# Kernel optimization log

Measured on AMD Instinct MI355X. Metric: run time of the kernel, lower is better.

The kernel has to match this reference:

```python
import jax, jax.numpy as jnp
import numpy as np
import math

B, S, D, H = 4, 2048, 1024, 16
HD = D // H  # head dim = 64


def setup_inputs() -> dict:
    key = jax.random.key(0)
    ks = jax.random.split(key, 8)
    queries = jax.random.normal(ks[0], (B, S, D), dtype=jnp.float32)
    keys = jax.random.normal(ks[1], (B, S, D), dtype=jnp.float32)
    values = jax.random.normal(ks[2], (B, S, D), dtype=jnp.float32)
    valid_lens = jnp.maximum(jax.random.randint(ks[3], (B,), 0, S), 1).astype(jnp.int64)
    scale = 1.0 / math.sqrt(D)
    Wq = jax.random.normal(ks[4], (H, D, HD), dtype=jnp.float32) * scale
    Wk = jax.random.normal(ks[5], (H, D, HD), dtype=jnp.float32) * scale
    Wv = jax.random.normal(ks[6], (H, D, HD), dtype=jnp.float32) * scale
    Wo = jax.random.normal(ks[7], (H * HD, D), dtype=jnp.float32) * scale
    return {"queries": queries, "keys": keys, "values": values,
            "valid_lens": valid_lens, "Wq": Wq, "Wk": Wk, "Wv": Wv, "Wo": Wo}


def reference(queries, keys, values, valid_lens, Wq, Wk, Wv, Wo):
    # Per-head projections, batched over heads: [B,S,D] x [H,D,HD] -> [B,H,S,HD]
    q = jnp.einsum('bsd,hde->bhse', queries, Wq)
    k = jnp.einsum('bsd,hde->bhse', keys, Wk)
    v = jnp.einsum('bsd,hde->bhse', values, Wv)
    # Scaled dot-product scores: [B,H,S,S]
    scores = jnp.einsum('bhse,bhte->bhst', q, k) / jnp.sqrt(jnp.float32(HD))
    # Padding mask only (causal=False default in the torch forward)
    pad = jnp.arange(S)[None, :] >= valid_lens[:, None]  # [B,S] True = masked
    scores = jnp.where(pad[:, None, None, :], -jnp.inf, scores)
    attn = jax.nn.softmax(scores, axis=-1)
    out = jnp.einsum('bhst,bhte->bhse', attn, v)  # [B,H,S,HD]
    out = out.transpose(0, 2, 1, 3).reshape(q.shape[0], S, H * HD)  # concat heads
    return out @ Wo
```

## Files before the change

kernel.cpp:

```cpp
#include <hip/hip_runtime.h>
#include <hip/hip_bf16.h>

typedef __bf16 bf16;
typedef __attribute__((ext_vector_type(8))) __bf16 bf16x8;
typedef __attribute__((ext_vector_type(4))) float f32x4;

#define DEV __device__ __forceinline__

DEV float fexp2(float x) {
#if __has_builtin(__builtin_amdgcn_exp2f)
  return __builtin_amdgcn_exp2f(x);
#else
  return exp2f(x);
#endif
}

DEV void gload_lds16(const void* g, void* l) {
  __builtin_amdgcn_global_load_lds(
      (__attribute__((address_space(1))) void*)(g),
      (__attribute__((address_space(3))) void*)(l), 16, 0, 0);
}

template <int N>
DEV void waitvm() { asm volatile("s_waitcnt vmcnt(%0)" ::"n"(N) : "memory"); }
DEV void fence() { asm volatile("" ::: "memory"); }
DEV void bar() { fence(); __builtin_amdgcn_s_barrier(); fence(); }

__global__ void k_cvt_all(const float* __restrict__ q, const float* __restrict__ k,
                          const float* __restrict__ v, const float* __restrict__ Wq,
                          const float* __restrict__ Wk, const float* __restrict__ Wv,
                          const float* __restrict__ Wo, bf16* __restrict__ qb,
                          bf16* __restrict__ kb, bf16* __restrict__ vb,
                          bf16* __restrict__ WqkvT, bf16* __restrict__ WoT) {
  const int bid = blockIdx.x;
  if (bid < 12288) {
    const int which = bid >> 12;
    const float* in = which == 0 ? q : which == 1 ? k : v;
    bf16* out = which == 0 ? qb : which == 1 ? kb : vb;
    const int i = (bid & 4095) * 256 + threadIdx.x;
    const float4* p = reinterpret_cast<const float4*>(in) + (size_t)i * 2;
    float4 a = p[0], b = p[1];
    bf16x8 o;
    o[0] = (bf16)a.x; o[1] = (bf16)a.y; o[2] = (bf16)a.z; o[3] = (bf16)a.w;
    o[4] = (bf16)b.x; o[5] = (bf16)b.y; o[6] = (bf16)b.z; o[7] = (bf16)b.w;
    *reinterpret_cast<bf16x8*>(out + (size_t)i * 8) = o;
  } else {
    const int idx = (bid - 12288) * 256 + threadIdx.x;
    const int which = idx >> 20, r = idx & ((1 << 20) - 1);
    if (which < 3) {
      const float* W = which == 0 ? Wq : which == 1 ? Wk : Wv;
      const int d = r & 1023, n = r >> 10;
      float val = W[((size_t)(n >> 6) << 16) + (size_t)d * 64 + (n & 63)];
      if (which == 0) val *= 0.180336880f;
      WqkvT[((size_t)which << 20) + r] = (bf16)val;
    } else {
      const int kk = r & 1023, n = r >> 10;
      WoT[r] = (bf16)Wo[(size_t)kk * 1024 + n];
    }
  }
}

DEV void stageA(const bf16* __restrict__ Am, bf16 (*lds)[64], int k0, int tid) {
  const int wv = tid >> 6;
#pragma unroll
  for (int l = 0; l < 2; ++l) {
    const int row = l * 64 + (tid >> 3);
    const int e = (((tid & 7) ^ (row & 7)) << 3);
    gload_lds16(Am + (size_t)row * 1024 + k0 + e,
                (char*)lds + l * 8192 + wv * 1024);
  }
}
DEV void stageBh(const bf16* __restrict__ Bt, bf16 (*lds)[64], int h, int k0, int tid) {
  const int wv = tid >> 6;
#pragma unroll
  for (int l = 0; l < 2; ++l) {
    const int row = h * 128 + l * 64 + (tid >> 3);
    const int e = (((tid & 7) ^ (row & 7)) << 3);
    gload_lds16(Bt + (size_t)row * 1024 + k0 + e,
                (char*)lds + h * 16384 + l * 8192 + wv * 1024);
  }
}
DEV bf16x8 ldsfrag(const bf16 (*lds)[64], int row, int kk, int lgrp) {
  const int ch = ((kk << 2) + lgrp) ^ (row & 7);
  return *reinterpret_cast<const bf16x8*>((const char*)&lds[row][0] + (ch << 4));
}

#define GEMM_KLOOP(Am, Bt, acc)                                               \
  stageA(Am, AsB[0], 0, tid);                                                 \
  stageBh(Bt, BsB[0], 0, 0, tid);                                             \
  stageBh(Bt, BsB[0], 1, 0, tid);                                             \
  stageBh(Bt, BsB[1], 0, 64, tid);                                            \
  stageBh(Bt, BsB[1], 1, 64, tid);                                            \
  waitvm<4>();                                                                \
  bar();                                                                      \
  int cur = 0;                                                                \
  for (int kt = 0; kt < NT; ++kt) {                                           \
    bf16x8 bfr[4][2], afr[2][2];                                              \
    _Pragma("unroll") for (int n = 0; n < 4; ++n)                             \
        _Pragma("unroll") for (int kk = 0; kk < 2; ++kk)                      \
            bfr[n][kk] = ldsfrag(BsB[cur], wn * 64 + n * 16 + lid, kk, lgrp); \
    _Pragma("unroll") for (int mi = 0; mi < 2; ++mi)                          \
        _Pragma("unroll") for (int kk = 0; kk < 2; ++kk)                      \
            afr[mi][kk] = ldsfrag(AsB[cur], wr * 64 + mi * 16 + lid, kk, lgrp); \
    if (kt + 1 < NT) stageA(Am, AsB[cur ^ 1], (kt + 1) * 64, tid);            \
    bar();                                                                    \
    __builtin_amdgcn_s_setprio(1);                                            \
    _Pragma("unroll") for (int mi = 0; mi < 2; ++mi)                          \
        _Pragma("unroll") for (int n = 0; n < 4; ++n)                         \
            _Pragma("unroll") for (int kk = 0; kk < 2; ++kk)                  \
                acc[mi][n] = __builtin_amdgcn_mfma_f32_16x16x32_bf16(         \
                    afr[mi][kk], bfr[n][kk], acc[mi][n], 0, 0, 0);            \
    __builtin_amdgcn_s_setprio(0);                                            \
    bar();                                                                    \
    _Pragma("unroll") for (int mi = 0; mi < 2; ++mi)                          \
        _Pragma("unroll") for (int kk = 0; kk < 2; ++kk)                      \
            afr[mi][kk] = ldsfrag(AsB[cur], wr * 64 + (2 + mi) * 16 + lid, kk, lgrp); \
    if (kt + 2 < NT) {                                                        \
      stageBh(Bt, BsB[cur], 0, (kt + 2) * 64, tid);                           \
      stageBh(Bt, BsB[cur], 1, (kt + 2) * 64, tid);                           \
    }                                                                         \
    bar();                                                                    \
    __builtin_amdgcn_s_setprio(1);                                            \
    _Pragma("unroll") for (int mi = 0; mi < 2; ++mi)                          \
        _Pragma("unroll") for (int n = 0; n < 4; ++n)                         \
            _Pragma("unroll") for (int kk = 0; kk < 2; ++kk)                  \
                acc[2 + mi][n] = __builtin_amdgcn_mfma_f32_16x16x32_bf16(     \
                    afr[mi][kk], bfr[n][kk], acc[2 + mi][n], 0, 0, 0);        \
    __builtin_amdgcn_s_setprio(0);                                            \
    if (kt < NT - 2) waitvm<4>();                                             \
    else if (kt == NT - 2) waitvm<0>();                                       \
    bar();                                                                    \
    cur ^= 1;                                                                 \
  }

__global__ __launch_bounds__(512, 2) void k_gemm_qkv(const bf16* __restrict__ qA,
                                                     const bf16* __restrict__ kA,
                                                     const bf16* __restrict__ vA,
                                                     const bf16* __restrict__ Wt,
                                                     bf16* __restrict__ Qh,
                                                     bf16* __restrict__ Kh,
                                                     bf16* __restrict__ Vt) {
  __shared__ __align__(16) bf16 AsB[2][128][64];
  __shared__ __align__(16) bf16 BsB[2][256][64];
  const int tid = threadIdx.x, lane = tid & 63, w = tid >> 6;
  const int lgrp = lane >> 4, lid = lane & 15;
  const int wr = w >> 2, wn = w & 3;
  const int bid0 = blockIdx.x;
  const int bid = (bid0 & 7) * 96 + (bid0 >> 3);
  const int proj = bid >> 8;
  const int local = bid & 255;
  const int mt = local >> 2, ntl = local & 3;
  const int m0 = mt * 128, n0 = ntl * 256;
  const bf16* A = proj == 0 ? qA : proj == 1 ? kA : vA;
  const bf16* Am = A + (size_t)m0 * 1024;
  const bf16* Bt = Wt + ((size_t)proj * 1024 + n0) * 1024;

  f32x4 acc[4][4] = {};
  constexpr int NT = 16;
  GEMM_KLOOP(Am, Bt, acc)

  const int hh = (n0 >> 6) + wn;
  if (proj == 0) {
#pragma unroll
    for (int mm = 0; mm < 4; ++mm) {
      const int rowb = m0 + wr * 64 + mm * 16 + lgrp * 4;
      const int bb = rowb >> 11, s = rowb & 2047;
#pragma unroll
      for (int n = 0; n < 4; ++n) {
        const int e = n * 16 + lid;
        bf16* dst = Qh + (((size_t)bb * 16 + hh) * 2048 + s) * 64 + e;
#pragma unroll
        for (int r = 0; r < 4; ++r) dst[(size_t)r * 64] = (bf16)acc[mm][n][r];
      }
    }
  } else if (proj == 1) {
#pragma unroll
    for (int mm = 0; mm < 4; ++mm) {
      const int rowb = m0 + wr * 64 + mm * 16 + lgrp * 4;
      const int bb = rowb >> 11, s = rowb & 2047;
#pragma unroll
      for (int n = 0; n < 4; ++n) {
        const int e = n * 16 + lid;
#pragma unroll
        for (int r = 0; r < 4; ++r) {
          const int sr = s + r;
          Kh[(((size_t)bb * 16 + hh) * 2048 + sr) * 64 + (e ^ ((sr & 7) << 3))] =
              (bf16)acc[mm][n][r];
        }
      }
    }
  } else {
#pragma unroll
    for (int mm = 0; mm < 4; ++mm) {
      const int rowb = m0 + wr * 64 + mm * 16 + lgrp * 4;
      const int bb = rowb >> 11, s = rowb & 2047;
#pragma unroll
      for (int n = 0; n < 4; ++n) {
        const int e = n * 16 + lid;
        union { bf16 hv[4]; uint2 u; } tmp;
#pragma unroll
        for (int r = 0; r < 4; ++r) tmp.hv[r] = (bf16)acc[mm][n][r];
        bf16* dst = Vt + (((size_t)bb * 16 + hh) * 64 + e) * 2048 + (s ^ ((e & 7) << 3));
        *reinterpret_cast<uint2*>(dst) = tmp.u;
      }
    }
  }
}

__global__ __launch_bounds__(512, 2) void k_gemm_out8(const bf16* __restrict__ A,
                                                      const bf16* __restrict__ Wo,
                                                      float* __restrict__ C) {
  __shared__ __align__(16) bf16 AsB[2][128][64];
  __shared__ __align__(16) bf16 BsB[2][256][64];
  const int tid = threadIdx.x, lane = tid & 63, w = tid >> 6;
  const int lgrp = lane >> 4, lid = lane & 15;
  const int wr = w >> 2, wn = w & 3;
  const int bid0 = blockIdx.x;
  const int bid = (bid0 & 7) * 32 + (bid0 >> 3);
  const int mt = bid >> 2, ntl = bid & 3;
  const int m0 = mt * 128, n0 = ntl * 256;
  const bf16* Am = A + (size_t)m0 * 1024;
  const bf16* Bt = Wo + (size_t)n0 * 1024;

  f32x4 acc[4][4] = {};
  constexpr int NT = 16;
  GEMM_KLOOP(Am, Bt, acc)

#pragma unroll
  for (int mm = 0; mm < 4; ++mm) {
    const int rowb = m0 + wr * 64 + mm * 16 + lgrp * 4;
#pragma unroll
    for (int n = 0; n < 4; ++n) {
      const int col = n0 + wn * 64 + n * 16 + lid;
#pragma unroll
      for (int r = 0; r < 4; ++r)
        C[(size_t)(rowb + r) * 1024 + col] = acc[mm][n][r];
    }
  }
}

__global__ __launch_bounds__(256, 3) void k_flash(const bf16* __restrict__ Qh,
                                                  const bf16* __restrict__ Ksw,
                                                  const bf16* __restrict__ Vsw,
                                                  const int* __restrict__ valid,
                                                  bf16* __restrict__ Ob) {
  __shared__ __align__(16) char Ks[2][8192];
  __shared__ __align__(16) char Vs[2][8192];
  __shared__ __align__(16) char Plds[4][4096];
  const int tid = threadIdx.x, lane = tid & 63, w = tid >> 6;
  const int lgrp = lane >> 4, lid = lane & 15;
  const int blk = blockIdx.x;
  const int qt = blk & 15, bh = blk >> 4;
  const int b = bh >> 4, h = bh & 15;
  const int s0 = qt * 128 + w * 32;
  const bf16* Qp = Qh + ((size_t)bh * 2048 + s0) * 64;
  const bf16* Kp = Ksw + (size_t)bh * 2048 * 64;
  const bf16* Vp = Vsw + (size_t)bh * 64 * 2048;
  const int vl = valid[b];
  const int nt = (vl + 63) >> 6;
  const int full = vl >> 6;

  const int sr0 = 16 * w + (lane >> 3), col8 = (lane & 7) * 8;

  gload_lds16(Kp + (size_t)sr0 * 64 + col8, &Ks[0][(16 * w) * 128]);
  gload_lds16(Kp + (size_t)(sr0 + 8) * 64 + col8, &Ks[0][(16 * w + 8) * 128]);
  gload_lds16(Vp + (size_t)sr0 * 2048 + col8, &Vs[0][(16 * w) * 128]);
  gload_lds16(Vp + (size_t)(sr0 + 8) * 2048 + col8, &Vs[0][(16 * w + 8) * 128]);

  bf16x8 aq[2][2];
#pragma unroll
  for (int g = 0; g < 2; ++g)
#pragma unroll
    for (int c = 0; c < 2; ++c)
      aq[g][c] = *reinterpret_cast<const bf16x8*>(Qp + (g * 16 + lid) * 64 + c * 32 + lgrp * 8);

  f32x4 Of[2][4] = {};
  float mrow[2] = {-1e30f, -1e30f};
  float lpart[2] = {0.f, 0.f};
  char* Pw = &Plds[w][0];
  float* PwF = (float*)Pw;
  const int pswz = (lid & 7) << 4;

  int cur = 0;
  for (int t = 0; t < nt; ++t) {
    const int t0 = t * 64;
    __syncthreads();
    if (t + 1 < nt) {
      const int t1 = t0 + 64;
      gload_lds16(Kp + (size_t)(t1 + sr0) * 64 + col8, &Ks[cur ^ 1][(16 * w) * 128]);
      gload_lds16(Kp + (size_t)(t1 + sr0 + 8) * 64 + col8, &Ks[cur ^ 1][(16 * w + 8) * 128]);
      gload_lds16(Vp + (size_t)sr0 * 2048 + t1 + col8, &Vs[cur ^ 1][(16 * w) * 128]);
      gload_lds16(Vp + (size_t)(sr0 + 8) * 2048 + t1 + col8, &Vs[cur ^ 1][(16 * w + 8) * 128]);
    }
    f32x4 sc[2][4] = {{}, {}};
#pragma unroll
    for (int kk = 0; kk < 2; ++kk) {
      bf16x8 bkh[4];
#pragma unroll
      for (int ct = 0; ct < 4; ++ct) {
        const int row = ct * 16 + lid;
        bkh[ct] = *reinterpret_cast<const bf16x8*>(
            &Ks[cur][row * 128] + ((kk * 64 + lgrp * 16) ^ ((row & 7) << 4)));
      }
#pragma unroll
      for (int g = 0; g < 2; ++g)
#pragma unroll
        for (int ct = 0; ct < 4; ++ct)
          sc[g][ct] = __builtin_amdgcn_mfma_f32_16x16x32_bf16(bkh[ct], aq[g][kk],
                                                              sc[g][ct], 0, 0, 0);
    }
    if (t >= full) {
#pragma unroll
      for (int ct = 0; ct < 4; ++ct)
#pragma unroll
        for (int r = 0; r < 4; ++r) {
          const bool m = (t0 + ct * 16 + lgrp * 4 + r) >= vl;
          sc[0][ct][r] = m ? -1e30f : sc[0][ct][r];
          sc[1][ct][r] = m ? -1e30f : sc[1][ct][r];
        }
    }
    float vm[2];
#pragma unroll
    for (int g = 0; g < 2; ++g) {
      float v = fmaxf(fmaxf(fmaxf(sc[g][0][0], sc[g][0][1]), fmaxf(sc[g][0][2], sc[g][0][3])),
                      fmaxf(fmaxf(sc[g][1][0], sc[g][1][1]), fmaxf(sc[g][1][2], sc[g][1][3])));
      v = fmaxf(v, fmaxf(fmaxf(fmaxf(sc[g][2][0], sc[g][2][1]), fmaxf(sc[g][2][2], sc[g][2][3])),
                         fmaxf(fmaxf(sc[g][3][0], sc[g][3][1]), fmaxf(sc[g][3][2], sc[g][3][3]))));
      vm[g] = v;
    }
    if (__any((vm[0] > mrow[0] + 8.f) | (vm[1] > mrow[1] + 8.f))) {
#pragma unroll
      for (int g = 0; g < 2; ++g) {
        float v = vm[g];
        v = fmaxf(v, __shfl_xor(v, 16));
        v = fmaxf(v, __shfl_xor(v, 32));
        float mnew = fmaxf(mrow[g], v);
        float scl = fexp2(mrow[g] - mnew);
        mrow[g] = mnew;
        lpart[g] *= scl;
        if (lgrp == 0) PwF[g * 512 + lid] = scl;
      }
      asm volatile("s_waitcnt lgkmcnt(0)" ::: "memory");
      f32x4 sq0 = *reinterpret_cast<const f32x4*>(PwF + lgrp * 4);
      f32x4 sq1 = *reinterpret_cast<const f32x4*>(PwF + 512 + lgrp * 4);
#pragma unroll
      for (int f = 0; f < 4; ++f)
#pragma unroll
        for (int r = 0; r < 4; ++r) {
          Of[0][f][r] *= sq0[r];
          Of[1][f][r] *= sq1[r];
        }
    }
#pragma unroll
    for (int g = 0; g < 2; ++g)
#pragma unroll
      for (int ct = 0; ct < 4; ++ct)
#pragma unroll
        for (int r = 0; r < 4; ++r)
          sc[g][ct][r] = fexp2(sc[g][ct][r] - mrow[g]);
#pragma unroll
    for (int g = 0; g < 2; ++g)
#pragma unroll
      for (int ct = 0; ct < 4; ++ct) {
        union { bf16 hv[2]; unsigned int u; } p0, p1;
        p0.hv[0] = (bf16)sc[g][ct][0]; p0.hv[1] = (bf16)sc[g][ct][1];
        p1.hv[0] = (bf16)sc[g][ct][2]; p1.hv[1] = (bf16)sc[g][ct][3];
        char* base = Pw + g * 2048 + lid * 128 + ((ct * 32 + lgrp * 8) ^ pswz);
        *reinterpret_cast<unsigned int*>(base) = p0.u;
        *reinterpret_cast<unsigned int*>(base + 4) = p1.u;
      }
    asm volatile("s_waitcnt lgkmcnt(0)" ::: "memory");
    bf16x8 pa[2][2];
#pragma unroll
    for (int g = 0; g < 2; ++g) {
      pa[g][0] = *reinterpret_cast<const bf16x8*>(Pw + g * 2048 + lid * 128 + ((lgrp * 16) ^ pswz));
      pa[g][1] = *reinterpret_cast<const bf16x8*>(Pw + g * 2048 + lid * 128 + ((64 + lgrp * 16) ^ pswz));
    }
#pragma unroll
    for (int f = 0; f < 4; ++f) {
      const int row = f * 16 + lid;
      const char* vb = &Vs[cur][row * 128];
      const int msk = (row & 7) << 4;
      bf16x8 bv0 = *reinterpret_cast<const bf16x8*>(vb + ((lgrp * 16) ^ msk));
      bf16x8 bv1 = *reinterpret_cast<const bf16x8*>(vb + ((64 + lgrp * 16) ^ msk));
      Of[0][f] = __builtin_amdgcn_mfma_f32_16x16x32_bf16(pa[0][0], bv0, Of[0][f], 0, 0, 0);
      Of[0][f] = __builtin_amdgcn_mfma_f32_16x16x32_bf16(pa[0][1], bv1, Of[0][f], 0, 0, 0);
      Of[1][f] = __builtin_amdgcn_mfma_f32_16x16x32_bf16(pa[1][0], bv0, Of[1][f], 0, 0, 0);
      Of[1][f] = __builtin_amdgcn_mfma_f32_16x16x32_bf16(pa[1][1], bv1, Of[1][f], 0, 0, 0);
    }
#pragma unroll
    for (int g = 0; g < 2; ++g)
      lpart[g] += ((sc[g][0][0] + sc[g][0][1]) + (sc[g][0][2] + sc[g][0][3])) +
                  ((sc[g][1][0] + sc[g][1][1]) + (sc[g][1][2] + sc[g][1][3])) +
                  ((sc[g][2][0] + sc[g][2][1]) + (sc[g][2][2] + sc[g][2][3])) +
                  ((sc[g][3][0] + sc[g][3][1]) + (sc[g][3][2] + sc[g][3][3]));
    cur ^= 1;
  }
#pragma unroll
  for (int g = 0; g < 2; ++g) {
    float l = lpart[g];
    l += __shfl_xor(l, 16);
    l += __shfl_xor(l, 32);
    if (lgrp == 0) PwF[g * 512 + lid] = 1.f / l;
  }
  asm volatile("s_waitcnt lgkmcnt(0)" ::: "memory");
  f32x4 iq0 = *reinterpret_cast<const f32x4*>(PwF + lgrp * 4);
  f32x4 iq1 = *reinterpret_cast<const f32x4*>(PwF + 512 + lgrp * 4);
  bf16* Op = Ob + ((size_t)b * 2048 + s0) * 1024 + h * 64;
#pragma unroll
  for (int r = 0; r < 4; ++r)
#pragma unroll
    for (int f = 0; f < 4; ++f) {
      Op[(size_t)(lgrp * 4 + r) * 1024 + f * 16 + lid] = (bf16)(Of[0][f][r] * iq0[r]);
      Op[(size_t)(16 + lgrp * 4 + r) * 1024 + f * 16 + lid] = (bf16)(Of[1][f][r] * iq1[r]);
    }
}

extern "C" void kernel_launch(void* const* d_in, const int* in_sizes, int n_in,
                              void* d_out, int out_size, void* d_ws, size_t ws_size,
                              hipStream_t stream) {
  const float* q = (const float*)d_in[0];
  const float* k = (const float*)d_in[1];
  const float* v = (const float*)d_in[2];
  const int* vl = (const int*)d_in[3];
  const float* Wq = (const float*)d_in[4];
  const float* Wk = (const float*)d_in[5];
  const float* Wv = (const float*)d_in[6];
  const float* Wo = (const float*)d_in[7];

  char* ws = (char*)d_ws;
  const size_t SZW = (size_t)1024 * 1024 * 2;
  const size_t SZT = (size_t)8192 * 1024 * 2;
  bf16* WqkvT = (bf16*)(ws);
  bf16* WoT = (bf16*)(ws + 3 * SZW);
  bf16* Qh  = (bf16*)(ws + 4 * SZW);
  bf16* Kh  = (bf16*)(ws + 4 * SZW + SZT);
  bf16* Vt  = (bf16*)(ws + 4 * SZW + 2 * SZT);
  bf16* qb  = (bf16*)(ws + 4 * SZW + 3 * SZT);
  bf16* kb  = (bf16*)(ws + 4 * SZW + 4 * SZT);
  bf16* vb  = (bf16*)(ws + 4 * SZW + 5 * SZT);
  bf16* attnb = qb;

  k_cvt_all<<<28672, 256, 0, stream>>>(q, k, v, Wq, Wk, Wv, Wo, qb, kb, vb,
                                       WqkvT, WoT);
  k_gemm_qkv<<<768, 512, 0, stream>>>(qb, kb, vb, WqkvT, Qh, Kh, Vt);
  k_flash<<<1024, 256, 0, stream>>>(Qh, Kh, Vt, vl, attnb);
  k_gemm_out8<<<256, 512, 0, stream>>>(attnb, WoT, (float*)d_out);
}
```

Before: 178.1 us.

## Halve QKV GEMM M-tile to 64 rows and double grid with higher occupancy

Shrinks the QKV projection GEMM tile from 128x256 to 64x256, rewriting the k-loop with a single-row A staging helper and two accumulator rows per warp instead of four. This doubles the grid to 1536 blocks and raises launch bounds to 4 blocks per CU, aiming to fill the GPU better and reduce register pressure. The trade-off is more redundant loads of the weight tiles per output element and lower arithmetic intensity per block.

```diff
diff --git a/kernel.cpp b/kernel.cpp
--- a/kernel.cpp
+++ b/kernel.cpp
@@ -69,6 +69,12 @@
     gload_lds16(Am + (size_t)row * 1024 + k0 + e,
                 (char*)lds + l * 8192 + wv * 1024);
   }
+}
+DEV void stageA64(const bf16* __restrict__ Am, bf16 (*lds)[64], int k0, int tid) {
+  const int row = tid >> 3;
+  const int e = (((tid & 7) ^ (row & 7)) << 3);
+  gload_lds16(Am + (size_t)row * 1024 + k0 + e,
+              (char*)lds + (tid >> 6) * 1024);
 }
 DEV void stageBh(const bf16* __restrict__ Bt, bf16 (*lds)[64], int h, int k0, int tid) {
   const int wv = tid >> 6;
@@ -133,37 +139,88 @@
     cur ^= 1;                                                                 \
   }
 
-__global__ __launch_bounds__(512, 2) void k_gemm_qkv(const bf16* __restrict__ qA,
+__global__ __launch_bounds__(512, 4) void k_gemm_qkv(const bf16* __restrict__ qA,
                                                      const bf16* __restrict__ kA,
                                                      const bf16* __restrict__ vA,
                                                      const bf16* __restrict__ Wt,
                                                      bf16* __restrict__ Qh,
                                                      bf16* __restrict__ Kh,
                                                      bf16* __restrict__ Vt) {
-  __shared__ __align__(16) bf16 AsB[2][128][64];
+  __shared__ __align__(16) bf16 AsB[2][64][64];
   __shared__ __align__(16) bf16 BsB[2][256][64];
   const int tid = threadIdx.x, lane = tid & 63, w = tid >> 6;
   const int lgrp = lane >> 4, lid = lane & 15;
   const int wr = w >> 2, wn = w & 3;
   const int bid0 = blockIdx.x;
-  const int bid = (bid0 & 7) * 96 + (bid0 >> 3);
-  const int proj = bid >> 8;
-  const int local = bid & 255;
+  const int bid = (bid0 & 7) * 192 + (bid0 >> 3);
+  const int proj = bid >> 9;
+  const int local = bid & 511;
   const int mt = local >> 2, ntl = local & 3;
-  const int m0 = mt * 128, n0 = ntl * 256;
+  const int m0 = mt * 64, n0 = ntl * 256;
   const bf16* A = proj == 0 ? qA : proj == 1 ? kA : vA;
   const bf16* Am = A + (size_t)m0 * 1024;
   const bf16* Bt = Wt + ((size_t)proj * 1024 + n0) * 1024;
 
-  f32x4 acc[4][4] = {};
+  f32x4 acc[2][4] = {};
   constexpr int NT = 16;
-  GEMM_KLOOP(Am, Bt, acc)
+
+  stageA64(Am, AsB[0], 0, tid);
+  stageBh(Bt, BsB[0], 0, 0, tid);
+  stageBh(Bt, BsB[0], 1, 0, tid);
+  stageBh(Bt, BsB[1], 0, 64, tid);
+  stageBh(Bt, BsB[1], 1, 64, tid);
+  waitvm<4>();
+  bar();
+
+  int cur = 0;
+  for (int kt = 0; kt < NT; ++kt) {
+    bf16x8 bfr[4][2], afr[2];
+#pragma unroll
+    for (int n = 0; n < 4; ++n)
+#pragma unroll
+      for (int kk = 0; kk < 2; ++kk)
+        bfr[n][kk] = ldsfrag(BsB[cur], wn * 64 + n * 16 + lid, kk, lgrp);
+#pragma unroll
+    for (int kk = 0; kk < 2; ++kk)
+      afr[kk] = ldsfrag(AsB[cur], wr * 32 + lid, kk, lgrp);
+    if (kt + 1 < NT) stageA64(Am, AsB[cur ^ 1], (kt + 1) * 64, tid);
+    bar();
+    __builtin_amdgcn_s_setprio(1);
+#pragma unroll
+    for (int n = 0; n < 4; ++n)
+#pragma unroll
+      for (int kk = 0; kk < 2; ++kk)
+        acc[0][n] = __builtin_amdgcn_mfma_f32_16x16x32_bf16(
+            afr[kk], bfr[n][kk], acc[0][n], 0, 0, 0);
+    __builtin_amdgcn_s_setprio(0);
+    bar();
+#pragma unroll
+    for (int kk = 0; kk < 2; ++kk)
+      afr[kk] = ldsfrag(AsB[cur], wr * 32 + 16 + lid, kk, lgrp);
+    if (kt + 2 < NT) {
+      stageBh(Bt, BsB[cur], 0, (kt + 2) * 64, tid);
+      stageBh(Bt, BsB[cur], 1, (kt + 2) * 64, tid);
+    }
+    bar();
+    __builtin_amdgcn_s_setprio(1);
+#pragma unroll
+    for (int n = 0; n < 4; ++n)
+#pragma unroll
+      for (int kk = 0; kk < 2; ++kk)
+        acc[1][n] = __builtin_amdgcn_mfma_f32_16x16x32_bf16(
+            afr[kk], bfr[n][kk], acc[1][n], 0, 0, 0);
+    __builtin_amdgcn_s_setprio(0);
+    if (kt < NT - 2) waitvm<4>();
+    else if (kt == NT - 2) waitvm<0>();
+    bar();
+    cur ^= 1;
+  }
 
   const int hh = (n0 >> 6) + wn;
   if (proj == 0) {
 #pragma unroll
-    for (int mm = 0; mm < 4; ++mm) {
-      const int rowb = m0 + wr * 64 + mm * 16 + lgrp * 4;
+    for (int mm = 0; mm < 2; ++mm) {
+      const int rowb = m0 + wr * 32 + mm * 16 + lgrp * 4;
       const int bb = rowb >> 11, s = rowb & 2047;
 #pragma unroll
       for (int n = 0; n < 4; ++n) {
@@ -175,8 +232,8 @@
     }
   } else if (proj == 1) {
 #pragma unroll
-    for (int mm = 0; mm < 4; ++mm) {
-      const int rowb = m0 + wr * 64 + mm * 16 + lgrp * 4;
+    for (int mm = 0; mm < 2; ++mm) {
+      const int rowb = m0 + wr * 32 + mm * 16 + lgrp * 4;
       const int bb = rowb >> 11, s = rowb & 2047;
 #pragma unroll
       for (int n = 0; n < 4; ++n) {
@@ -191,8 +248,8 @@
     }
   } else {
 #pragma unroll
-    for (int mm = 0; mm < 4; ++mm) {
-      const int rowb = m0 + wr * 64 + mm * 16 + lgrp * 4;
+    for (int mm = 0; mm < 2; ++mm) {
+      const int rowb = m0 + wr * 32 + mm * 16 + lgrp * 4;
       const int bb = rowb >> 11, s = rowb & 2047;
 #pragma unroll
       for (int n = 0; n < 4; ++n) {
@@ -443,7 +500,7 @@
 
   k_cvt_all<<<28672, 256, 0, stream>>>(q, k, v, Wq, Wk, Wv, Wo, qb, kb, vb,
                                        WqkvT, WoT);
-  k_gemm_qkv<<<768, 512, 0, stream>>>(qb, kb, vb, WqkvT, Qh, Kh, Vt);
+  k_gemm_qkv<<<1536, 512, 0, stream>>>(qb, kb, vb, WqkvT, Qh, Kh, Vt);
   k_flash<<<1024, 256, 0, stream>>>(Qh, Kh, Vt, vl, attnb);
   k_gemm_out8<<<256, 512, 0, stream>>>(attnb, WoT, (float*)d_out);
 }
```

Result: no change. 178.1 us (-0.0%).
